# Optimization experiments

Measured on AMD Instinct MI355X. Metric: run time of the kernel, lower is better.

The kernel has to match this reference:

```python
import jax, jax.numpy as jnp
import numpy as np

N_NODES = 50000
N_EDGES = 800000
DIM = 128
NUM_GRAPHS = 512
NEG_SLOPE_ATT = 0.2   # GATConv attention leaky_relu slope
NEG_SLOPE_ACT = 0.01  # F.leaky_relu default in forward
EPS = 1e-16


def setup_inputs() -> dict:
    key = jax.random.key(0)
    ks = jax.random.split(key, 10)
    x = jax.random.normal(ks[0], (N_NODES, DIM), dtype=jnp.float32)
    edge_index = jax.random.randint(ks[1], (2, N_EDGES), 0, N_NODES, dtype=jnp.int64)
    batch = jnp.sort(jax.random.randint(ks[2], (N_NODES,), 0, NUM_GRAPHS, dtype=jnp.int64))
    s = 1.0 / np.sqrt(DIM)
    inp = {"x": x, "edge_index": edge_index, "batch": batch}
    for i in range(3):
        inp[f"W{i}"] = jax.random.uniform(ks[3 + i], (DIM, DIM), jnp.float32, -s, s)
        a = jax.random.uniform(ks[6 + i], (2, DIM), jnp.float32, -s, s)
        inp[f"a_src{i}"] = a[0]
        inp[f"a_dst{i}"] = a[1]
    return inp


def _gat_conv(x, src, dst, W, a_src, a_dst):
    # h = lin(x); heads=1, concat, bias=False
    h = x @ W.T                                     # [N, D]
    e = jax.nn.leaky_relu((h @ a_src)[src] + (h @ a_dst)[dst], NEG_SLOPE_ATT)  # [E]
    # segment softmax over destination neighborhoods
    m = jax.ops.segment_max(e, dst, num_segments=N_NODES)
    ee = jnp.exp(e - m[dst])
    z = jax.ops.segment_sum(ee, dst, num_segments=N_NODES)
    alpha = ee / (z[dst] + EPS)                     # [E]
    return jax.ops.segment_sum(h[src] * alpha[:, None], dst, num_segments=N_NODES)


def reference(x, edge_index, batch, W0, a_src0, a_dst0, W1, a_src1, a_dst1, W2, a_src2, a_dst2):
    loops = jnp.arange(N_NODES, dtype=edge_index.dtype)
    src = jnp.concatenate([edge_index[0], loops])  # add_self_loops=True
    dst = jnp.concatenate([edge_index[1], loops])
    x = _gat_conv(x, src, dst, W0, a_src0, a_dst0)
    x = _gat_conv(x, src, dst, W1, a_src1, a_dst1)
    x = jax.nn.leaky_relu(x, NEG_SLOPE_ACT)
    x = _gat_conv(x, src, dst, W2, a_src2, a_dst2)
    # global_add_pool
    return jax.ops.segment_sum(x, batch, num_segments=NUM_GRAPHS)
```

## Files before the change

### kernel.cpp

```cpp
#include <hip/hip_runtime.h>
#include <hip/hip_bf16.h>
#include <hip/hip_fp16.h>
#include <math.h>

#define NN 50000
#define NE 800000
#define DD 128
#define NG 512
#define NSA 0.2f
#define NSB 0.01f
#define EPS 1e-16f
#define CAP 61

typedef _Float16 half8 __attribute__((ext_vector_type(8)));
typedef float    floatx4 __attribute__((ext_vector_type(4)));

__global__ void init_kernel(unsigned int* __restrict__ cnt, float* __restrict__ out,
                            const float* __restrict__ W0, const float* __restrict__ W1,
                            const float* __restrict__ W2, __half* __restrict__ w16) {
    int i = blockIdx.x * 256 + threadIdx.x;
    if (i < NN) cnt[i] = 0u;
    if (i < NG * DD) out[i] = 0.f;
    if (i < 3 * DD * DD) {
        int layer = i / (DD * DD), idx = i % (DD * DD);
        const float* Ws = (layer == 0) ? W0 : (layer == 1) ? W1 : W2;
        w16[i] = __float2half(Ws[idx]);
    }
}

#define BM 64
__device__ __forceinline__ void gemm_mfma_body(
        const float* __restrict__ X, const __half* __restrict__ W16,
        const float* __restrict__ a_src, const float* __restrict__ a_dst,
        __half* __restrict__ H16, float* __restrict__ as_, float* __restrict__ ad_,
        int row0, __half (*tile)[136]) {
    int t    = threadIdx.x;
    int wave = t >> 6;
    int lane = t & 63;
    int quad = lane >> 4;
    int mrow = lane & 15;
    int gl = min(row0 + wave * 16 + mrow, NN - 1);

    half8 afrag[4];
    #pragma unroll
    for (int kc = 0; kc < 4; ++kc) {
        int k = kc * 32 + quad * 8;
        float4 u0 = *(const float4*)&X[(size_t)gl * DD + k];
        float4 u1 = *(const float4*)&X[(size_t)gl * DD + k + 4];
        half8 a;
        a[0] = (_Float16)u0.x; a[1] = (_Float16)u0.y;
        a[2] = (_Float16)u0.z; a[3] = (_Float16)u0.w;
        a[4] = (_Float16)u1.x; a[5] = (_Float16)u1.y;
        a[6] = (_Float16)u1.z; a[7] = (_Float16)u1.w;
        afrag[kc] = a;
    }

    floatx4 acc[8] = {};
    #pragma unroll
    for (int ct = 0; ct < 8; ++ct) {
        #pragma unroll
        for (int kc = 0; kc < 4; ++kc) {
            half8 b = *(const half8*)&W16[(size_t)(ct * 16 + mrow) * DD + kc * 32 + quad * 8];
            acc[ct] = __builtin_amdgcn_mfma_f32_16x16x32_f16(afrag[kc], b, acc[ct], 0, 0, 0);
        }
    }
    #pragma unroll
    for (int ct = 0; ct < 8; ++ct) {
        #pragma unroll
        for (int reg = 0; reg < 4; ++reg)
            tile[wave * 16 + quad * 4 + reg][ct * 16 + mrow] = __float2half(acc[ct][reg]);
    }
    __syncthreads();

    int tx = t & 15;
    int ty = t >> 4;
    float asv[8], adv[8];
    #pragma unroll
    for (int c = 0; c < 8; ++c) {
        asv[c] = a_src[tx * 8 + c];
        adv[c] = a_dst[tx * 8 + c];
    }
    #pragma unroll
    for (int r = 0; r < 4; ++r) {
        int row = ty * 4 + r;
        int gr = row0 + row;
        float4 raw = *(const float4*)&tile[row][tx * 8];
        const __half2* q = (const __half2*)&raw;
        float2 c01 = __half22float2(q[0]);
        float2 c23 = __half22float2(q[1]);
        float2 c45 = __half22float2(q[2]);
        float2 c67 = __half22float2(q[3]);
        float hv[8] = {c01.x, c01.y, c23.x, c23.y, c45.x, c45.y, c67.x, c67.y};
        float ps = 0.f, pd = 0.f;
        #pragma unroll
        for (int c = 0; c < 8; ++c) {
            ps += hv[c] * asv[c];
            pd += hv[c] * adv[c];
        }
        #pragma unroll
        for (int off = 8; off >= 1; off >>= 1) {
            ps += __shfl_xor(ps, off);
            pd += __shfl_xor(pd, off);
        }
        if (gr < NN) {
            if (tx == 0) { as_[gr] = ps; ad_[gr] = pd; }
            *(float4*)&H16[(size_t)gr * DD + tx * 8] = raw;
        }
    }
}

__global__ __launch_bounds__(256, 8) void fat_kernel(
        const float* __restrict__ X, const __half* __restrict__ W16,
        const float* __restrict__ a_src, const float* __restrict__ a_dst,
        __half* __restrict__ H16, float* __restrict__ as_, float* __restrict__ ad_,
        const int* __restrict__ esrc, const int* __restrict__ edst,
        unsigned int* __restrict__ cnt, unsigned short* __restrict__ slots) {
    __shared__ __half tile[BM][136];
    int bx = blockIdx.x;
    if (bx & 1) {
        int i = (bx >> 1) * 256 + threadIdx.x;
        if (i < NE / 4) {
            int4 s4 = ((const int4*)esrc)[i];
            int4 d4 = ((const int4*)edst)[i];
            int k0 = (int)atomicAdd(&cnt[d4.x], 1u);
            int k1 = (int)atomicAdd(&cnt[d4.y], 1u);
            int k2 = (int)atomicAdd(&cnt[d4.z], 1u);
            int k3 = (int)atomicAdd(&cnt[d4.w], 1u);
            if (k0 < CAP) slots[((size_t)d4.x << 6) + k0] = (unsigned short)s4.x;
            if (k1 < CAP) slots[((size_t)d4.y << 6) + k1] = (unsigned short)s4.y;
            if (k2 < CAP) slots[((size_t)d4.z << 6) + k2] = (unsigned short)s4.z;
            if (k3 < CAP) slots[((size_t)d4.w << 6) + k3] = (unsigned short)s4.w;
        }
        return;
    }
    gemm_mfma_body(X, W16, a_src, a_dst, H16, as_, ad_, (bx >> 1) * BM, tile);
}

__device__ inline void fma_h8(float4& a0, float4& a1, float p, const float4& raw) {
    const __half2* q = (const __half2*)&raw;
    float2 c;
    c = __half22float2(q[0]); a0.x += p * c.x; a0.y += p * c.y;
    c = __half22float2(q[1]); a0.z += p * c.x; a0.w += p * c.y;
    c = __half22float2(q[2]); a1.x += p * c.x; a1.y += p * c.y;
    c = __half22float2(q[3]); a1.z += p * c.x; a1.w += p * c.y;
}

__device__ __forceinline__ void agg_batch4(
        int row0, int wid, int lane,
        const __half* __restrict__ H16, const float* __restrict__ as_,
        const float* __restrict__ ad_, const unsigned int* __restrict__ cnt,
        const unsigned short* __restrict__ slots,
        float (*p_sh)[4][64], int (*s_sh)[4][64], __half (*ytile)[136],
        int apply_lrelu) {
    int nodes[4], deg[4];
    float adn[4], ll[4];

    int cv[4];
    #pragma unroll
    for (int it = 0; it < 4; ++it) {
        nodes[it] = row0 + it * 4 + wid;
        cv[it] = (int)cnt[nodes[it]];
    }
    int sl[4];
    #pragma unroll
    for (int it = 0; it < 4; ++it)
        sl[it] = (int)slots[((size_t)nodes[it] << 6) + lane];
    #pragma unroll
    for (int it = 0; it < 4; ++it) adn[it] = ad_[nodes[it]];
    int svv[4];
    #pragma unroll
    for (int it = 0; it < 4; ++it) {
        int dr = min(cv[it], CAP);
        deg[it] = dr + 1;
        svv[it] = (lane < dr) ? sl[it] : nodes[it];
        s_sh[wid][it][lane] = svv[it];
    }
    float av[4];
    #pragma unroll
    for (int it = 0; it < 4; ++it) av[it] = as_[svv[it]];
    #pragma unroll
    for (int it = 0; it < 4; ++it) {
        float e = -1e30f;
        if (lane < deg[it]) {
            float ev = av[it] + adn[it];
            e = (ev > 0.f) ? ev : NSA * ev;
        }
        float m = e;
        #pragma unroll
        for (int off = 32; off >= 1; off >>= 1) m = fmaxf(m, __shfl_xor(m, off));
        float pv = (lane < deg[it]) ? __expf(e - m) : 0.f;
        p_sh[wid][it][lane] = pv;
        float l = pv;
        #pragma unroll
        for (int off = 32; off >= 1; off >>= 1) l += __shfl_xor(l, off);
        ll[it] = l;
    }
    __builtin_amdgcn_wave_barrier();

    int g = lane >> 4;
    int d = lane & 15;
    int   dg = (g == 0) ? deg[0] : (g == 1) ? deg[1] : (g == 2) ? deg[2] : deg[3];
    float lg = (g == 0) ? ll[0]  : (g == 1) ? ll[1]  : (g == 2) ? ll[2]  : ll[3];
    const int*    srow = s_sh[wid][g];
    const float*  prow = p_sh[wid][g];
    const float4* H4   = (const float4*)H16;
    float4 a0 = {0,0,0,0}, a1 = {0,0,0,0};
    int jm = dg & ~7;
    for (int j = 0; j < jm; j += 8) {
        int s0 = srow[j+0], s1 = srow[j+1], s2 = srow[j+2], s3 = srow[j+3];
        int s4 = srow[j+4], s5 = srow[j+5], s6 = srow[j+6], s7 = srow[j+7];
        float p0 = prow[j+0], p1 = prow[j+1], p2 = prow[j+2], p3 = prow[j+3];
        float p4 = prow[j+4], p5 = prow[j+5], p6 = prow[j+6], p7 = prow[j+7];
        float4 r0 = H4[(size_t)s0 * 16 + d];
        float4 r1 = H4[(size_t)s1 * 16 + d];
        float4 r2 = H4[(size_t)s2 * 16 + d];
        float4 r3 = H4[(size_t)s3 * 16 + d];
        float4 r4 = H4[(size_t)s4 * 16 + d];
        float4 r5 = H4[(size_t)s5 * 16 + d];
        float4 r6 = H4[(size_t)s6 * 16 + d];
        float4 r7 = H4[(size_t)s7 * 16 + d];
        fma_h8(a0, a1, p0, r0);
        fma_h8(a0, a1, p1, r1);
        fma_h8(a0, a1, p2, r2);
        fma_h8(a0, a1, p3, r3);
        fma_h8(a0, a1, p4, r4);
        fma_h8(a0, a1, p5, r5);
        fma_h8(a0, a1, p6, r6);
        fma_h8(a0, a1, p7, r7);
    }
    int rem = dg - jm;
    #pragma unroll
    for (int k = 0; k < 7; ++k) {
        if (k < rem) {
            int s = srow[jm + k];
            float p = prow[jm + k];
            float4 r = H4[(size_t)s * 16 + d];
            fma_h8(a0, a1, p, r);
        }
    }
    float inv = 1.f / (lg + EPS);
    float4 o0, o1;
    o0.x = a0.x * inv; o0.y = a0.y * inv; o0.z = a0.z * inv; o0.w = a0.w * inv;
    o1.x = a1.x * inv; o1.y = a1.y * inv; o1.z = a1.z * inv; o1.w = a1.w * inv;
    if (apply_lrelu) {
        o0.x = (o0.x > 0.f) ? o0.x : NSB * o0.x;
        o0.y = (o0.y > 0.f) ? o0.y : NSB * o0.y;
        o0.z = (o0.z > 0.f) ? o0.z : NSB * o0.z;
        o0.w = (o0.w > 0.f) ? o0.w : NSB * o0.w;
        o1.x = (o1.x > 0.f) ? o1.x : NSB * o1.x;
        o1.y = (o1.y > 0.f) ? o1.y : NSB * o1.y;
        o1.z = (o1.z > 0.f) ? o1.z : NSB * o1.z;
        o1.w = (o1.w > 0.f) ? o1.w : NSB * o1.w;
    }
    __half2 hh[4];
    hh[0] = __floats2half2_rn(o0.x, o0.y);
    hh[1] = __floats2half2_rn(o0.z, o0.w);
    hh[2] = __floats2half2_rn(o1.x, o1.y);
    hh[3] = __floats2half2_rn(o1.z, o1.w);
    *(float4*)&ytile[g * 4 + wid][d * 8] = *(float4*)hh;
}

__global__ __launch_bounds__(256, 6) void agg_gemm_kernel(
        const __half* __restrict__ H_in, const float* __restrict__ as_in,
        const float* __restrict__ ad_in, const unsigned int* __restrict__ cnt,
        const unsigned short* __restrict__ slots,
        const __half* __restrict__ W16, const float* __restrict__ a_src,
        const float* __restrict__ a_dst, __half* __restrict__ H_out,
        float* __restrict__ as_out, float* __restrict__ ad_out, int apply_lrelu) {
    __shared__ float  p_sh[4][4][64];
    __shared__ int    s_sh[4][4][64];
    __shared__ __half ytile[16][136];
    int t = threadIdx.x;
    int wid = t >> 6, lane = t & 63;
    int row0 = blockIdx.x * 16;

    agg_batch4(row0, wid, lane, H_in, as_in, ad_in, cnt, slots, p_sh, s_sh, ytile,
               apply_lrelu);
    __syncthreads();

    int quad = lane >> 4, mrow = lane & 15;
    half8 afrag[4];
    #pragma unroll
    for (int kc = 0; kc < 4; ++kc)
        afrag[kc] = *(const half8*)&ytile[mrow][kc * 32 + quad * 8];
    __syncthreads();

    floatx4 acc[2] = {};
    #pragma unroll
    for (int cc = 0; cc < 2; ++cc) {
        int ct = wid * 2 + cc;
        #pragma unroll
        for (int kc = 0; kc < 4; ++kc) {
            half8 b = *(const half8*)&W16[(size_t)(ct * 16 + mrow) * DD + kc * 32 + quad * 8];
            acc[cc] = __builtin_amdgcn_mfma_f32_16x16x32_f16(afrag[kc], b, acc[cc], 0, 0, 0);
        }
    }
    #pragma unroll
    for (int cc = 0; cc < 2; ++cc) {
        int ct = wid * 2 + cc;
        #pragma unroll
        for (int reg = 0; reg < 4; ++reg)
            ytile[quad * 4 + reg][ct * 16 + mrow] = __float2half(acc[cc][reg]);
    }
    __syncthreads();

    int row = t >> 4, cg = t & 15;
    int gr = row0 + row;
    float4 raw = *(const float4*)&ytile[row][cg * 8];
    const __half2* q = (const __half2*)&raw;
    float2 c01 = __half22float2(q[0]);
    float2 c23 = __half22float2(q[1]);
    float2 c45 = __half22float2(q[2]);
    float2 c67 = __half22float2(q[3]);
    float hv[8] = {c01.x, c01.y, c23.x, c23.y, c45.x, c45.y, c67.x, c67.y};
    float ps = 0.f, pd = 0.f;
    #pragma unroll
    for (int c = 0; c < 8; ++c) {
        ps += hv[c] * a_src[cg * 8 + c];
        pd += hv[c] * a_dst[cg * 8 + c];
    }
    #pragma unroll
    for (int off = 8; off >= 1; off >>= 1) {
        ps += __shfl_xor(ps, off);
        pd += __shfl_xor(pd, off);
    }
    if (cg == 0) { as_out[gr] = ps; ad_out[gr] = pd; }
    *(float4*)&H_out[(size_t)gr * DD + cg * 8] = raw;
}

__global__ __launch_bounds__(256, 6) void agg_pool_kernel(
        const __half* __restrict__ H_in, const float* __restrict__ as_in,
        const float* __restrict__ ad_in, const unsigned int* __restrict__ cnt,
        const unsigned short* __restrict__ slots,
        const int* __restrict__ batch, float* __restrict__ out) {
    __shared__ float  p_sh[4][4][64];
    __shared__ int    s_sh[4][4][64];
    __shared__ __half ytile[16][136];
    int t = threadIdx.x;
    int wid = t >> 6, lane = t & 63;
    int row0 = blockIdx.x * 16;

    agg_batch4(row0, wid, lane, H_in, as_in, ad_in, cnt, slots, p_sh, s_sh, ytile, 0);
    __syncthreads();

    int rh = t >> 7;
    int d  = t & 127;
    int r0 = rh * 8;
    float acc = 0.f;
    int g = batch[row0 + r0];
    #pragma unroll
    for (int r = 0; r < 8; ++r) {
        int n = row0 + r0 + r;
        int gn = batch[n];
        if (gn != g) {
            atomicAdd(&out[(size_t)g * DD + d], acc);
            acc = 0.f;
            g = gn;
        }
        acc += __half2float(ytile[r0 + r][d]);
    }
    atomicAdd(&out[(size_t)g * DD + d], acc);
}

extern "C" void kernel_launch(void* const* d_in, const int* in_sizes, int n_in,
                              void* d_out, int out_size, void* d_ws, size_t ws_size,
                              hipStream_t stream) {
    const float* x      = (const float*)d_in[0];
    const int*   ei     = (const int*)d_in[1];
    const int*   batch  = (const int*)d_in[2];
    const int*   src    = ei;
    const int*   dst    = ei + NE;
    float* out = (float*)d_out;

    size_t off = 0;
    auto carve = [&](size_t bytes) {
        void* p = (char*)d_ws + off;
        off += (bytes + 255) & ~(size_t)255;
        return p;
    };
    __half* h16a  = (__half*)carve((size_t)NN * DD * 2);
    __half* h16b  = (__half*)carve((size_t)NN * DD * 2);
    float*  as_a  = (float*)carve((size_t)NN * 4);
    float*  ad_a  = (float*)carve((size_t)NN * 4);
    float*  as_b  = (float*)carve((size_t)NN * 4);
    float*  ad_b  = (float*)carve((size_t)NN * 4);
    unsigned int*   cnt   = (unsigned int*)carve((size_t)NN * 4);
    unsigned short* slots = (unsigned short*)carve((size_t)NN * 64 * 2);
    __half* w16   = (__half*)carve((size_t)3 * DD * DD * 2);

    const int gemm_blocks = (NN + BM - 1) / BM;
    const int fat_blocks  = gemm_blocks * 2;
    const int fuse_blocks = NN / 16;
    const int init_blocks = (NG * DD + 255) / 256;

    const float* W0  = (const float*)d_in[3];
    const float* av0 = (const float*)d_in[4];
    const float* ad0 = (const float*)d_in[5];
    const float* av1 = (const float*)d_in[7];
    const float* ad1 = (const float*)d_in[8];
    const float* av2 = (const float*)d_in[10];
    const float* ad2 = (const float*)d_in[11];

    init_kernel<<<init_blocks, 256, 0, stream>>>(cnt, out, W0,
                                                 (const float*)d_in[6],
                                                 (const float*)d_in[9], w16);
    fat_kernel<<<fat_blocks, 256, 0, stream>>>(
        x, w16, av0, ad0, h16a, as_a, ad_a, src, dst, cnt, slots);

    agg_gemm_kernel<<<fuse_blocks, 256, 0, stream>>>(
        h16a, as_a, ad_a, cnt, slots, w16 + (size_t)1 * DD * DD, av1, ad1,
        h16b, as_b, ad_b, 0);
    agg_gemm_kernel<<<fuse_blocks, 256, 0, stream>>>(
        h16b, as_b, ad_b, cnt, slots, w16 + (size_t)2 * DD * DD, av2, ad2,
        h16a, as_a, ad_a, 1);

    agg_pool_kernel<<<fuse_blocks, 256, 0, stream>>>(h16a, as_a, ad_a, cnt, slots,
                                                     batch, out);
}
```

Baseline: 251.0 us.

## Double-buffer neighbor gathers and overlap them with the segment softmax

The neighbor aggregation now issues gathers for the first two 8-neighbor chunks into two register banks before the softmax runs, then alternates between consuming one bank and refilling it. The softmax is restructured so each 16-lane group reduces its own row using float4 loads from shared memory, with shuffles over 16 lanes instead of 64, and chunk padding reads zero probabilities. This hides gather latency behind the softmax and arithmetic, at the cost of many more live registers, so the occupancy hint is lowered from 6 to 4 blocks per CU.

```diff
diff --git a/kernel.cpp b/kernel.cpp
--- a/kernel.cpp
+++ b/kernel.cpp
@@ -145,6 +145,32 @@
     c = __half22float2(q[3]); a1.z += p * c.x; a1.w += p * c.y;
 }
 
+#define LDCH(Rp, cc) do {                                                     \
+    int4 _i0 = *(const int4*)&srow[(cc) * 8];                                 \
+    int4 _i1 = *(const int4*)&srow[(cc) * 8 + 4];                             \
+    Rp##0 = H4[(size_t)_i0.x * 16 + d];                                       \
+    Rp##1 = H4[(size_t)_i0.y * 16 + d];                                       \
+    Rp##2 = H4[(size_t)_i0.z * 16 + d];                                       \
+    Rp##3 = H4[(size_t)_i0.w * 16 + d];                                       \
+    Rp##4 = H4[(size_t)_i1.x * 16 + d];                                       \
+    Rp##5 = H4[(size_t)_i1.y * 16 + d];                                       \
+    Rp##6 = H4[(size_t)_i1.z * 16 + d];                                       \
+    Rp##7 = H4[(size_t)_i1.w * 16 + d];                                       \
+} while (0)
+
+#define EAT(Rp, cc) do {                                                      \
+    float4 _q0 = *(const float4*)&prow[(cc) * 8];                             \
+    float4 _q1 = *(const float4*)&prow[(cc) * 8 + 4];                         \
+    fma_h8(a0, a1, _q0.x, Rp##0);                                             \
+    fma_h8(a0, a1, _q0.y, Rp##1);                                             \
+    fma_h8(a0, a1, _q0.z, Rp##2);                                             \
+    fma_h8(a0, a1, _q0.w, Rp##3);                                             \
+    fma_h8(a0, a1, _q1.x, Rp##4);                                             \
+    fma_h8(a0, a1, _q1.y, Rp##5);                                             \
+    fma_h8(a0, a1, _q1.z, Rp##6);                                             \
+    fma_h8(a0, a1, _q1.w, Rp##7);                                             \
+} while (0)
+
 __device__ __forceinline__ void agg_batch4(
         int row0, int wid, int lane,
         const __half* __restrict__ H16, const float* __restrict__ as_,
@@ -153,7 +179,7 @@
         float (*p_sh)[4][64], int (*s_sh)[4][64], __half (*ytile)[136],
         int apply_lrelu) {
     int nodes[4], deg[4];
-    float adn[4], ll[4];
+    float adn[4];
 
     int cv[4];
     #pragma unroll
@@ -178,6 +204,22 @@
     float av[4];
     #pragma unroll
     for (int it = 0; it < 4; ++it) av[it] = as_[svv[it]];
+    __builtin_amdgcn_wave_barrier();
+
+    int g = lane >> 4;
+    int d = lane & 15;
+    int dg = (g == 0) ? deg[0] : (g == 1) ? deg[1] : (g == 2) ? deg[2] : deg[3];
+    const int*   srow = s_sh[wid][g];
+    float*       prow = p_sh[wid][g];
+    const float4* H4  = (const float4*)H16;
+    int nch = (dg + 7) >> 3;
+
+    float4 A0, A1, A2, A3, A4, A5, A6, A7;
+    float4 B0, B1, B2, B3, B4, B5, B6, B7;
+    LDCH(A, 0);
+    LDCH(B, 1);
+    __builtin_amdgcn_sched_barrier(0);
+
     #pragma unroll
     for (int it = 0; it < 4; ++it) {
         float e = -1e30f;
@@ -185,60 +227,37 @@
             float ev = av[it] + adn[it];
             e = (ev > 0.f) ? ev : NSA * ev;
         }
-        float m = e;
-        #pragma unroll
-        for (int off = 32; off >= 1; off >>= 1) m = fmaxf(m, __shfl_xor(m, off));
-        float pv = (lane < deg[it]) ? __expf(e - m) : 0.f;
-        p_sh[wid][it][lane] = pv;
-        float l = pv;
-        #pragma unroll
-        for (int off = 32; off >= 1; off >>= 1) l += __shfl_xor(l, off);
-        ll[it] = l;
+        p_sh[wid][it][lane] = e;
     }
     __builtin_amdgcn_wave_barrier();
 
-    int g = lane >> 4;
-    int d = lane & 15;
-    int   dg = (g == 0) ? deg[0] : (g == 1) ? deg[1] : (g == 2) ? deg[2] : deg[3];
-    float lg = (g == 0) ? ll[0]  : (g == 1) ? ll[1]  : (g == 2) ? ll[2]  : ll[3];
-    const int*    srow = s_sh[wid][g];
-    const float*  prow = p_sh[wid][g];
-    const float4* H4   = (const float4*)H16;
-    float4 a0 = {0,0,0,0}, a1 = {0,0,0,0};
-    int jm = dg & ~7;
-    for (int j = 0; j < jm; j += 8) {
-        int s0 = srow[j+0], s1 = srow[j+1], s2 = srow[j+2], s3 = srow[j+3];
-        int s4 = srow[j+4], s5 = srow[j+5], s6 = srow[j+6], s7 = srow[j+7];
-        float p0 = prow[j+0], p1 = prow[j+1], p2 = prow[j+2], p3 = prow[j+3];
-        float p4 = prow[j+4], p5 = prow[j+5], p6 = prow[j+6], p7 = prow[j+7];
-        float4 r0 = H4[(size_t)s0 * 16 + d];
-        float4 r1 = H4[(size_t)s1 * 16 + d];
-        float4 r2 = H4[(size_t)s2 * 16 + d];
-        float4 r3 = H4[(size_t)s3 * 16 + d];
-        float4 r4 = H4[(size_t)s4 * 16 + d];
-        float4 r5 = H4[(size_t)s5 * 16 + d];
-        float4 r6 = H4[(size_t)s6 * 16 + d];
-        float4 r7 = H4[(size_t)s7 * 16 + d];
-        fma_h8(a0, a1, p0, r0);
-        fma_h8(a0, a1, p1, r1);
-        fma_h8(a0, a1, p2, r2);
-        fma_h8(a0, a1, p3, r3);
-        fma_h8(a0, a1, p4, r4);
-        fma_h8(a0, a1, p5, r5);
-        fma_h8(a0, a1, p6, r6);
-        fma_h8(a0, a1, p7, r7);
-    }
-    int rem = dg - jm;
-    #pragma unroll
-    for (int k = 0; k < 7; ++k) {
-        if (k < rem) {
-            int s = srow[jm + k];
-            float p = prow[jm + k];
-            float4 r = H4[(size_t)s * 16 + d];
-            fma_h8(a0, a1, p, r);
-        }
-    }
-    float inv = 1.f / (lg + EPS);
+    float4 ev4 = *(const float4*)&prow[d * 4];
+    float m = fmaxf(fmaxf(ev4.x, ev4.y), fmaxf(ev4.z, ev4.w));
+    #pragma unroll
+    for (int off = 8; off >= 1; off >>= 1) m = fmaxf(m, __shfl_xor(m, off));
+    float4 pv;
+    pv.x = __expf(ev4.x - m);
+    pv.y = __expf(ev4.y - m);
+    pv.z = __expf(ev4.z - m);
+    pv.w = __expf(ev4.w - m);
+    *(float4*)&prow[d * 4] = pv;
+    float lsum = pv.x + pv.y + pv.z + pv.w;
+    #pragma unroll
+    for (int off = 8; off >= 1; off >>= 1) lsum += __shfl_xor(lsum, off);
+    __builtin_amdgcn_wave_barrier();
+
+    float4 a0 = {0, 0, 0, 0}, a1 = {0, 0, 0, 0};
+    int c = 0;
+    while (true) {
+        EAT(A, c);
+        if (c + 2 < nch) LDCH(A, c + 2);
+        if (c + 1 >= nch) break;
+        EAT(B, c + 1);
+        if (c + 3 < nch) LDCH(B, c + 3);
+        c += 2;
+    }
+
+    float inv = 1.f / (lsum + EPS);
     float4 o0, o1;
     o0.x = a0.x * inv; o0.y = a0.y * inv; o0.z = a0.z * inv; o0.w = a0.w * inv;
     o1.x = a1.x * inv; o1.y = a1.y * inv; o1.z = a1.z * inv; o1.w = a1.w * inv;
@@ -260,7 +279,7 @@
     *(float4*)&ytile[g * 4 + wid][d * 8] = *(float4*)hh;
 }
 
-__global__ __launch_bounds__(256, 6) void agg_gemm_kernel(
+__global__ __launch_bounds__(256, 4) void agg_gemm_kernel(
         const __half* __restrict__ H_in, const float* __restrict__ as_in,
         const float* __restrict__ ad_in, const unsigned int* __restrict__ cnt,
         const unsigned short* __restrict__ slots,
@@ -328,7 +347,7 @@
     *(float4*)&H_out[(size_t)gr * DD + cg * 8] = raw;
 }
 
-__global__ __launch_bounds__(256, 6) void agg_pool_kernel(
+__global__ __launch_bounds__(256, 4) void agg_pool_kernel(
         const __half* __restrict__ H_in, const float* __restrict__ as_in,
         const float* __restrict__ ad_in, const unsigned int* __restrict__ cnt,
         const unsigned short* __restrict__ slots,
```

New measurement: 378.0 us. 50.6% more time.
